# Performance work log

Hardware: AMD Instinct MI355X
Metric: run time of the kernel (lower is better)

## Reference

```python
import jax, jax.numpy as jnp
import numpy as np

T, B, E, H = 2048, 2, 1024, 16
D = E // H  # head_dim = 64

def setup_inputs() -> dict:
    key = jax.random.key(0)
    ks = jax.random.split(key, 9)
    s = 1.0 / np.sqrt(E)
    return {
        "query": jax.random.normal(ks[0], (T, B, E), dtype=jnp.float32),
        "Wq": jax.random.normal(ks[1], (E, E), dtype=jnp.float32) * s,
        "bq": jax.random.normal(ks[2], (E,), dtype=jnp.float32) * 0.02,
        "Wk": jax.random.normal(ks[3], (E, E), dtype=jnp.float32) * s,
        "bk": jax.random.normal(ks[4], (E,), dtype=jnp.float32) * 0.02,
        "Wv": jax.random.normal(ks[5], (E, E), dtype=jnp.float32) * s,
        "bv": jax.random.normal(ks[6], (E,), dtype=jnp.float32) * 0.02,
        "Wo": jax.random.normal(ks[7], (E, E), dtype=jnp.float32) * s,
        "bo": jax.random.normal(ks[8], (E,), dtype=jnp.float32) * 0.02,
    }

def reference(query, Wq, bq, Wk, bk, Wv, bv, Wo, bo):
    # query: [T, B, E] (fairseq Time x Batch x Channel layout)
    t, b, e = query.shape
    scaling = D ** -0.5
    q = (query @ Wq.T + bq) * scaling          # [T,B,E], scaled like fairseq
    k = query @ Wk.T + bk                      # self-attention: k,v from query
    v = query @ Wv.T + bv
    # split heads: [T,B,H,D]
    q = q.reshape(t, b, H, D)
    k = k.reshape(t, b, H, D)
    v = v.reshape(t, b, H, D)
    # attn weights: [B,H,T(tgt),S(src)]
    scores = jnp.einsum("tbhd,sbhd->bhts", q, k)
    probs = jax.nn.softmax(scores, axis=-1)
    # attend: [T,B,H,D] -> [T,B,E]
    ctx = jnp.einsum("bhts,sbhd->tbhd", probs, v).reshape(t, b, e)
    return ctx @ Wo.T + bo                     # [T,B,E]
```

## Files before the change

kernel.cpp:

```cpp
#include <hip/hip_runtime.h>
#include <hip/hip_bf16.h>
#include <math.h>

#define TT 2048
#define BB 2
#define EE 1024
#define HH 16
#define DD 64
#define RR (TT*BB)

typedef __bf16 bf16x8 __attribute__((ext_vector_type(8)));
typedef float  floatx4 __attribute__((ext_vector_type(4)));

__device__ __forceinline__ unsigned short f2b(float f) {
    union { float f; unsigned u; } x{f};
    return (unsigned short)((x.u + 0x7FFFu + ((x.u >> 16) & 1u)) >> 16);
}
__device__ __forceinline__ float b2f_lo(unsigned u) {
    union { unsigned u; float f; } x{u << 16}; return x.f;
}
__device__ __forceinline__ float b2f_hi(unsigned u) {
    union { unsigned u; float f; } x{u & 0xffff0000u}; return x.f;
}

__device__ __forceinline__ float exp2_fast(float x) {
    return __builtin_amdgcn_exp2f(x);
}

typedef const __attribute__((address_space(1))) unsigned int as1_u32;
typedef __attribute__((address_space(3))) unsigned int as3_u32;
__device__ __forceinline__ void gload16(const void* g, void* l) {
    __builtin_amdgcn_global_load_lds((as1_u32*)g, (as3_u32*)l, 16, 0, 0);
}

#define SCALE_Q 0.18033688011112042f

__device__ __forceinline__ int swz(int r) {
    return (r & 7) ^ (((r >> 3) & 3) << 1);
}

__global__ __launch_bounds__(256)
void pack_bf16(const float* __restrict__ x,  const float* __restrict__ wq,
               const float* __restrict__ wk, const float* __restrict__ wv,
               const float* __restrict__ wo, unsigned short* __restrict__ base,
               unsigned short* __restrict__ wob)
{
    const size_t M4 = (size_t)4 << 20, M7 = (size_t)7 << 20;
    const size_t e0 = ((size_t)blockIdx.x * 256 + threadIdx.x) * 8;
    const float* src;
    unsigned short* dst;
    if (e0 < M4) {
        src = x + e0; dst = base + e0;
    } else if (e0 < M7) {
        const int seg = (int)((e0 >> 20) - 4);
        const float* wsrc[3] = {wq, wk, wv};
        src = wsrc[seg] + (e0 & ((1u << 20) - 1));
        dst = base + e0;
    } else {
        src = wo + (e0 - M7); dst = wob + (e0 - M7);
    }
    const float4 a = *(const float4*)src;
    const float4 b = *(const float4*)(src + 4);
    union { unsigned short u[8]; uint4 v; } p;
    p.u[0] = f2b(a.x); p.u[1] = f2b(a.y); p.u[2] = f2b(a.z); p.u[3] = f2b(a.w);
    p.u[4] = f2b(b.x); p.u[5] = f2b(b.y); p.u[6] = f2b(b.z); p.u[7] = f2b(b.w);
    *(uint4*)dst = p.v;
}

template<int MODE>
__global__ __launch_bounds__(256)
void gemm_mfma(const unsigned short* __restrict__ A,
               const unsigned short* __restrict__ Bw,
               const float* __restrict__ b0, const float* __restrict__ b1,
               const float* __restrict__ b2,
               void* __restrict__ out0, void* __restrict__ out1,
               void* __restrict__ out2)
{
    constexpr int BM = 128;
    constexpr int BN = (MODE == 0) ? 128 : 64;
    constexpr int MT = 4;
    constexpr int NT = (MODE == 0) ? 4 : 2;
    constexpr int RA = BM / 32;
    constexpr int RB = BN / 32;
    constexpr int ABYTES = BM * 128;
    constexpr int BUFB   = (BM + BN) * 128;
    __shared__ __align__(16) unsigned char smem[2 * BUFB];

    const int tid  = threadIdx.x;
    const int w    = tid >> 6;
    const int lane = tid & 63;
    const int quad = lane >> 4;
    const int l15  = lane & 15;
    const int wm   = w & 1;
    const int wn   = w >> 1;
    const int i0   = blockIdx.x * BM;
    const int j0   = blockIdx.y * BN;

    const unsigned short* ga[RA];
    const unsigned short* gb[RB];
    #pragma unroll
    for (int r = 0; r < RA; ++r) {
        const int slot = r * 256 + tid;
        const int row  = slot >> 3;
        const int gc   = (slot & 7) ^ swz(row);
        ga[r] = A + (size_t)(i0 + row) * EE + gc * 8;
    }
    #pragma unroll
    for (int r = 0; r < RB; ++r) {
        const int slot = r * 256 + tid;
        const int row  = slot >> 3;
        const int gc   = (slot & 7) ^ swz(row);
        gb[r] = Bw + (size_t)(j0 + row) * EE + gc * 8;
    }

    int ofsA[2][MT], ofsB[2][NT];
    #pragma unroll
    for (int mt = 0; mt < MT; ++mt) {
        const int row = wm * 64 + mt * 16 + l15;
        #pragma unroll
        for (int ks = 0; ks < 2; ++ks)
            ofsA[ks][mt] = row * 64 + (((ks * 4 + quad) ^ swz(row)) << 3);
    }
    #pragma unroll
    for (int nt = 0; nt < NT; ++nt) {
        const int col = wn * (BN / 2) + nt * 16 + l15;
        #pragma unroll
        for (int ks = 0; ks < 2; ++ks)
            ofsB[ks][nt] = col * 64 + (((ks * 4 + quad) ^ swz(col)) << 3);
    }

    floatx4 acc[MT][NT];
    #pragma unroll
    for (int mt = 0; mt < MT; ++mt)
        #pragma unroll
        for (int nt = 0; nt < NT; ++nt)
            acc[mt][nt] = (floatx4){0.f, 0.f, 0.f, 0.f};

    {
        unsigned short* nA = (unsigned short*)(smem);
        unsigned short* nB = (unsigned short*)(smem + ABYTES);
        #pragma unroll
        for (int r = 0; r < RA; ++r)
            gload16(ga[r], nA + (r * 256 + w * 64) * 8);
        #pragma unroll
        for (int r = 0; r < RB; ++r)
            gload16(gb[r], nB + (r * 256 + w * 64) * 8);
    }

    int cur = 0;
    for (int kk = 0; kk < EE; kk += 64) {
        asm volatile("s_waitcnt vmcnt(0)" ::: "memory");
        __builtin_amdgcn_s_barrier();

        if (kk + 64 < EE) {
            unsigned short* nA = (unsigned short*)(smem + (cur ^ 1) * BUFB);
            unsigned short* nB = (unsigned short*)(smem + (cur ^ 1) * BUFB + ABYTES);
            #pragma unroll
            for (int r = 0; r < RA; ++r)
                gload16(ga[r] + kk + 64, nA + (r * 256 + w * 64) * 8);
            #pragma unroll
            for (int r = 0; r < RB; ++r)
                gload16(gb[r] + kk + 64, nB + (r * 256 + w * 64) * 8);
        }
        __builtin_amdgcn_sched_barrier(0);

        const unsigned short* lA = (const unsigned short*)(smem + cur * BUFB);
        const unsigned short* lB = (const unsigned short*)(smem + cur * BUFB + ABYTES);

        bf16x8 af[2][MT], bfr[2][NT];
        #pragma unroll
        for (int ks = 0; ks < 2; ++ks) {
            #pragma unroll
            for (int mt = 0; mt < MT; ++mt)
                af[ks][mt] = __builtin_bit_cast(bf16x8, *(const uint4*)&lA[ofsA[ks][mt]]);
            #pragma unroll
            for (int nt = 0; nt < NT; ++nt)
                bfr[ks][nt] = __builtin_bit_cast(bf16x8, *(const uint4*)&lB[ofsB[ks][nt]]);
        }

        #pragma unroll
        for (int ks = 0; ks < 2; ++ks)
            #pragma unroll
            for (int mt = 0; mt < MT; ++mt)
                #pragma unroll
                for (int nt = 0; nt < NT; ++nt)
                    acc[mt][nt] = __builtin_amdgcn_mfma_f32_16x16x32_bf16(
                        af[ks][mt], bfr[ks][nt], acc[mt][nt], 0, 0, 0);

        cur ^= 1;
    }

    if (MODE == 1) {
        float* dst = (float*)out0;
        #pragma unroll
        for (int nt = 0; nt < NT; ++nt) {
            const int j = j0 + wn * 32 + nt * 16 + l15;
            const float bb = b0[j];
            #pragma unroll
            for (int mt = 0; mt < MT; ++mt) {
                const int i = i0 + wm * 64 + mt * 16 + quad * 4;
                #pragma unroll
                for (int r2 = 0; r2 < 4; ++r2)
                    dst[(size_t)(i + r2) * EE + j] = acc[mt][nt][r2] + bb;
            }
        }
    } else {
        const int which = j0 >> 10;
        const float scale = (which == 0) ? SCALE_Q : 1.0f;
        const float* bias = (which == 0) ? b0 : (which == 1) ? b1 : b2;
        if (which < 2) {
            unsigned short* dst = (unsigned short*)(which == 0 ? out0 : out1);
            #pragma unroll
            for (int nt = 0; nt < NT; ++nt) {
                const int j = (j0 & 1023) + wn * 64 + nt * 16 + l15;
                const int h = j >> 6, d = j & 63;
                const float bb = bias[j];
                #pragma unroll
                for (int mt = 0; mt < MT; ++mt) {
                    const int i = i0 + wm * 64 + mt * 16 + quad * 4;
                    #pragma unroll
                    for (int r2 = 0; r2 < 4; ++r2) {
                        const int ii = i + r2;
                        const int t = ii >> 1, b = ii & 1;
                        dst[((size_t)(b * HH + h) * TT + t) * DD + d] =
                            f2b((acc[mt][nt][r2] + bb) * scale);
                    }
                }
            }
        } else {
            __syncthreads();
            unsigned short* tr = (unsigned short*)smem + (size_t)w * 64 * 68;
            #pragma unroll
            for (int nt = 0; nt < NT; ++nt) {
                const int jl = nt * 16 + l15;
                const float bb = bias[(j0 & 1023) + wn * 64 + jl];
                #pragma unroll
                for (int mt = 0; mt < MT; ++mt) {
                    const int il0 = mt * 16 + quad * 4;
                    ushort4 h4;
                    h4.x = f2b(acc[mt][nt][0] + bb);
                    h4.y = f2b(acc[mt][nt][1] + bb);
                    h4.z = f2b(acc[mt][nt][2] + bb);
                    h4.w = f2b(acc[mt][nt][3] + bb);
                    *(ushort4*)&tr[jl * 68 + il0] = h4;
                }
            }
            __syncthreads();
            const int jg = (j0 & 1023) + wn * 64 + lane;
            const int h = jg >> 6, d = jg & 63;
            const int tb = (i0 + wm * 64) >> 1;
            const unsigned short* rp = tr + (size_t)lane * 68;
            unsigned short* dstV = (unsigned short*)out2;
            #pragma unroll
            for (int g = 0; g < 4; ++g) {
                union { unsigned short u[8]; uint4 v; } pe, po;
                #pragma unroll
                for (int k = 0; k < 8; ++k) {
                    pe.u[k] = rp[(g * 8 + k) * 2];
                    po.u[k] = rp[(g * 8 + k) * 2 + 1];
                }
                *(uint4*)&dstV[((size_t)(0 * HH + h) * DD + d) * TT + tb + g * 8] = pe.v;
                *(uint4*)&dstV[((size_t)(1 * HH + h) * DD + d) * TT + tb + g * 8] = po.v;
            }
        }
    }
}

__global__ __launch_bounds__(256)
void attn_mfma(const unsigned short* __restrict__ Q,
               const unsigned short* __restrict__ K,
               const unsigned short* __restrict__ Vt,
               unsigned short* __restrict__ cpart,
               float* __restrict__ lsumbuf)
{
    __shared__ __align__(16) unsigned short ring[3][2][64 * 64];

    const int tid  = threadIdx.x;
    const int w    = tid >> 6;
    const int lane = tid & 63;
    const int quad = lane >> 4;
    const int l15  = lane & 15;
    const int bh   = blockIdx.x;
    const int tt   = blockIdx.y;
    const int half = blockIdx.z;

    const unsigned short* Qh = Q  + (size_t)bh * TT * DD;
    const unsigned short* Kh = K  + (size_t)bh * TT * DD;
    const unsigned short* Vh = Vt + (size_t)bh * DD * TT;

    const int q0w  = tt * 128 + w * 32;
    const int key0 = half * 1024;

    bf16x8 qf[2][2];
    #pragma unroll
    for (int qn = 0; qn < 2; ++qn)
        #pragma unroll
        for (int kd = 0; kd < 2; ++kd)
            qf[qn][kd] = __builtin_bit_cast(bf16x8,
                *(const uint4*)&Qh[(size_t)(q0w + qn * 16 + l15) * DD + kd * 32 + quad * 8]);

    const unsigned short* kg[4];
    #pragma unroll
    for (int r = 0; r < 4; ++r) {
        const int slot = r * 256 + tid;
        const int row  = slot >> 3;
        const int gc   = (slot & 7) ^ swz(row);
        kg[r] = Kh + (size_t)(key0 + row) * DD + gc * 8;
    }
    const unsigned short* vg[4];
    #pragma unroll
    for (int r = 0; r < 4; ++r) {
        const int s512 = (r & 1) * 256 + tid;
        const int rowd = s512 >> 3;
        const int gc   = (s512 & 7) ^ swz(rowd);
        vg[r] = Vh + (size_t)rowd * TT + key0 + (r >> 1) * 64 + gc * 8;
    }

    int ofsKA[4][2], ofsVB[4][2];
    #pragma unroll
    for (int mt = 0; mt < 4; ++mt) {
        const int row = ((mt >> 1) << 5) + ((l15 >> 2) << 3) + ((mt & 1) << 2) + (l15 & 3);
        #pragma unroll
        for (int kd = 0; kd < 2; ++kd)
            ofsKA[mt][kd] = row * 64 + (((kd * 4 + quad) ^ swz(row)) << 3);
    }
    #pragma unroll
    for (int dn = 0; dn < 4; ++dn) {
        const int row = dn * 16 + l15;
        #pragma unroll
        for (int ks = 0; ks < 2; ++ks)
            ofsVB[dn][ks] = row * 64 + (((ks * 4 + quad) ^ swz(row)) << 3);
    }

    floatx4 cacc[4][2];
    #pragma unroll
    for (int dn = 0; dn < 4; ++dn)
        #pragma unroll
        for (int qn = 0; qn < 2; ++qn)
            cacc[dn][qn] = (floatx4){0.f, 0.f, 0.f, 0.f};
    float rs[2] = {0.f, 0.f};

#define STAGE_ATTN(s)  do {                                                     \
        const int p_ = (s) & 1;                                                 \
        const size_t ko_ = (size_t)((s) >> 1) * 128;                            \
        unsigned short* kd_ = &ring[(s) % 3][0][0];                             \
        unsigned short* vd_ = &ring[(s) % 3][1][0];                             \
        gload16(kg[2 * p_]     + ko_ * DD, kd_ + (size_t)(0 * 256 + w * 64) * 8); \
        gload16(kg[2 * p_ + 1] + ko_ * DD, kd_ + (size_t)(1 * 256 + w * 64) * 8); \
        gload16(vg[2 * p_]     + ko_,      vd_ + (size_t)(0 * 256 + w * 64) * 8); \
        gload16(vg[2 * p_ + 1] + ko_,      vd_ + (size_t)(1 * 256 + w * 64) * 8); \
    } while (0)

    STAGE_ATTN(0);
    STAGE_ATTN(1);

    #pragma unroll
    for (int step = 0; step < 16; ++step) {
        const int rb = step % 3;
        if (step < 15) asm volatile("s_waitcnt vmcnt(4)" ::: "memory");
        else           asm volatile("s_waitcnt vmcnt(0)" ::: "memory");
        __builtin_amdgcn_s_barrier();
        if (step + 2 < 16) STAGE_ATTN(step + 2);
        __builtin_amdgcn_sched_barrier(0);
        __builtin_amdgcn_s_setprio(1);

        const unsigned short* ksub = &ring[rb][0][0];
        const unsigned short* vsub = &ring[rb][1][0];

        uint2 pk[4][2];
        #pragma unroll
        for (int mt = 0; mt < 4; ++mt) {
            const bf16x8 ka0 = __builtin_bit_cast(bf16x8, *(const uint4*)&ksub[ofsKA[mt][0]]);
            const bf16x8 ka1 = __builtin_bit_cast(bf16x8, *(const uint4*)&ksub[ofsKA[mt][1]]);
            #pragma unroll
            for (int qn = 0; qn < 2; ++qn) {
                floatx4 s = (floatx4){0.f, 0.f, 0.f, 0.f};
                s = __builtin_amdgcn_mfma_f32_16x16x32_bf16(ka0, qf[qn][0], s, 0, 0, 0);
                s = __builtin_amdgcn_mfma_f32_16x16x32_bf16(ka1, qf[qn][1], s, 0, 0, 0);
                const float p0 = exp2_fast(s[0]);
                const float p1 = exp2_fast(s[1]);
                const float p2 = exp2_fast(s[2]);
                const float p3 = exp2_fast(s[3]);
                rs[qn] += (p0 + p1) + (p2 + p3);
                union { __hip_bfloat162 h2[2]; uint2 u; } c;
                c.h2[0] = __float22bfloat162_rn(make_float2(p0, p1));
                c.h2[1] = __float22bfloat162_rn(make_float2(p2, p3));
                pk[mt][qn] = c.u;
            }
        }
        bf16x8 pa[2][2];
        #pragma unroll
        for (int qn = 0; qn < 2; ++qn) {
            union { uint2 d[2]; uint4 v; } a0, a1;
            a0.d[0] = pk[0][qn]; a0.d[1] = pk[1][qn];
            a1.d[0] = pk[2][qn]; a1.d[1] = pk[3][qn];
            pa[qn][0] = __builtin_bit_cast(bf16x8, a0.v);
            pa[qn][1] = __builtin_bit_cast(bf16x8, a1.v);
        }
        #pragma unroll
        for (int dn = 0; dn < 4; ++dn) {
            const bf16x8 vb0 = __builtin_bit_cast(bf16x8, *(const uint4*)&vsub[ofsVB[dn][0]]);
            const bf16x8 vb1 = __builtin_bit_cast(bf16x8, *(const uint4*)&vsub[ofsVB[dn][1]]);
            #pragma unroll
            for (int qn = 0; qn < 2; ++qn) {
                cacc[dn][qn] = __builtin_amdgcn_mfma_f32_16x16x32_bf16(pa[qn][0], vb0, cacc[dn][qn], 0, 0, 0);
                cacc[dn][qn] = __builtin_amdgcn_mfma_f32_16x16x32_bf16(pa[qn][1], vb1, cacc[dn][qn], 0, 0, 0);
            }
        }
        __builtin_amdgcn_s_setprio(0);
    }
#undef STAGE_ATTN

    const int b = bh / HH, hh = bh % HH;
    float rsw[2];
    #pragma unroll
    for (int qn = 0; qn < 2; ++qn) {
        float t = rs[qn];
        t += __shfl_xor(t, 16);
        t += __shfl_xor(t, 32);
        rsw[qn] = t;
    }
    unsigned short* cp = cpart + (size_t)half * RR * EE;
    #pragma unroll
    for (int qn = 0; qn < 2; ++qn) {
        #pragma unroll
        for (int dn = 0; dn < 4; ++dn) {
            const int e = hh * 64 + dn * 16 + l15;
            #pragma unroll
            for (int j = 0; j < 4; ++j) {
                const int t = q0w + qn * 16 + quad * 4 + j;
                cp[(size_t)(t * BB + b) * EE + e] = f2b(cacc[dn][qn][j]);
            }
        }
    }
    if (quad == 0) {
        lsumbuf[(half * BB * HH + bh) * TT + q0w + 0 * 16 + l15] = rsw[0];
        lsumbuf[(half * BB * HH + bh) * TT + q0w + 1 * 16 + l15] = rsw[1];
    }
}

__global__ __launch_bounds__(256)
void combine(const unsigned short* __restrict__ cpart,
             const float* __restrict__ lsumbuf,
             unsigned short* __restrict__ cb)
{
    const int gid = blockIdx.x * 256 + threadIdx.x;
    const int e0 = (gid & 127) * 8;
    const int r  = gid >> 7;
    const int t = r >> 1, b = r & 1;
    const int h = e0 >> 6;
    const int bh = b * HH + h;
    const float inv = 1.0f /
        (lsumbuf[bh * TT + t] + lsumbuf[(BB * HH + bh) * TT + t]);
    const uint4 c0 = *(const uint4*)&cpart[(size_t)r * EE + e0];
    const uint4 c1 = *(const uint4*)&cpart[(size_t)RR * EE + (size_t)r * EE + e0];
    const unsigned u0[4] = {c0.x, c0.y, c0.z, c0.w};
    const unsigned u1[4] = {c1.x, c1.y, c1.z, c1.w};
    union { unsigned u[4]; uint4 v; } o;
    #pragma unroll
    for (int k = 0; k < 4; ++k) {
        const float lo = (b2f_lo(u0[k]) + b2f_lo(u1[k])) * inv;
        const float hi = (b2f_hi(u0[k]) + b2f_hi(u1[k])) * inv;
        union { __hip_bfloat162 h2; unsigned u; } pk;
        pk.h2 = __float22bfloat162_rn(make_float2(lo, hi));
        o.u[k] = pk.u;
    }
    *(uint4*)&cb[(size_t)r * EE + e0] = o.v;
}

extern "C" void kernel_launch(void* const* d_in, const int* in_sizes, int n_in,
                              void* d_out, int out_size, void* d_ws, size_t ws_size,
                              hipStream_t stream)
{
    const float* x  = (const float*)d_in[0];
    const float* Wq = (const float*)d_in[1];
    const float* bq = (const float*)d_in[2];
    const float* Wk = (const float*)d_in[3];
    const float* bk = (const float*)d_in[4];
    const float* Wv = (const float*)d_in[5];
    const float* bv = (const float*)d_in[6];
    const float* Wo = (const float*)d_in[7];
    const float* bo = (const float*)d_in[8];
    float* out = (float*)d_out;

    const size_t M1 = (size_t)1 << 20;
    unsigned short* base  = (unsigned short*)d_ws;
    unsigned short* xb    = base;
    unsigned short* wqkv  = base + 4 * M1;
    unsigned short* cpart = base;
    unsigned short* qb    = base + 8 * M1;
    unsigned short* kb    = base + 12 * M1;
    unsigned short* vtb   = base + 16 * M1;
    unsigned short* cb    = base + 20 * M1;
    unsigned short* wob   = base + 24 * M1;
    float*          lsum  = (float*)(base + 25 * M1);

    dim3 blk(256);

    pack_bf16<<<dim3(4096), blk, 0, stream>>>(x, Wq, Wk, Wv, Wo, base, wob);

    gemm_mfma<0><<<dim3(RR / 128, 3072 / 128), blk, 0, stream>>>(
        xb, wqkv, bq, bk, bv, qb, kb, vtb);

    attn_mfma<<<dim3(BB * HH, TT / 128, 2), blk, 0, stream>>>(qb, kb, vtb, cpart, lsum);

    combine<<<dim3(RR * EE / 8 / 256), blk, 0, stream>>>(cpart, lsum, cb);

    gemm_mfma<1><<<dim3(RR / 128, EE / 64), blk, 0, stream>>>(
        cb, wob, bo, nullptr, nullptr, out, nullptr, nullptr);
}
```

Measured before the change: 179.9 us.

## Drop split-KV attention and fuse normalization into attention epilogue

Each attention block now walks all 2048 keys instead of half, and the separate combine kernel and partial-output buffers are removed. The softmax normalization by the row sum happens in the attention epilogue through lane shuffles before the bf16 store. This removes one launch plus the write and reread of two partial context tensors. The cost is half as many attention blocks (512 instead of 1024), so fewer waves are available to fill the GPU's compute units.

```diff
diff --git a/kernel.cpp b/kernel.cpp
--- a/kernel.cpp
+++ b/kernel.cpp
@@ -270,8 +270,7 @@
 void attn_mfma(const unsigned short* __restrict__ Q,
                const unsigned short* __restrict__ K,
                const unsigned short* __restrict__ Vt,
-               unsigned short* __restrict__ cpart,
-               float* __restrict__ lsumbuf)
+               unsigned short* __restrict__ cb)
 {
     __shared__ __align__(16) unsigned short ring[3][2][64 * 64];
 
@@ -282,14 +281,12 @@
     const int l15  = lane & 15;
     const int bh   = blockIdx.x;
     const int tt   = blockIdx.y;
-    const int half = blockIdx.z;
 
     const unsigned short* Qh = Q  + (size_t)bh * TT * DD;
     const unsigned short* Kh = K  + (size_t)bh * TT * DD;
     const unsigned short* Vh = Vt + (size_t)bh * DD * TT;
 
     const int q0w  = tt * 128 + w * 32;
-    const int key0 = half * 1024;
 
     bf16x8 qf[2][2];
     #pragma unroll
@@ -305,7 +302,7 @@
         const int slot = r * 256 + tid;
         const int row  = slot >> 3;
         const int gc   = (slot & 7) ^ swz(row);
-        kg[r] = Kh + (size_t)(key0 + row) * DD + gc * 8;
+        kg[r] = Kh + (size_t)row * DD + gc * 8;
     }
     const unsigned short* vg[4];
     #pragma unroll
@@ -313,7 +310,7 @@
         const int s512 = (r & 1) * 256 + tid;
         const int rowd = s512 >> 3;
         const int gc   = (s512 & 7) ^ swz(rowd);
-        vg[r] = Vh + (size_t)rowd * TT + key0 + (r >> 1) * 64 + gc * 8;
+        vg[r] = Vh + (size_t)rowd * TT + (r >> 1) * 64 + gc * 8;
     }
 
     int ofsKA[4][2], ofsVB[4][2];
@@ -355,12 +352,12 @@
     STAGE_ATTN(1);
 
     #pragma unroll
-    for (int step = 0; step < 16; ++step) {
+    for (int step = 0; step < 32; ++step) {
         const int rb = step % 3;
-        if (step < 15) asm volatile("s_waitcnt vmcnt(4)" ::: "memory");
+        if (step < 31) asm volatile("s_waitcnt vmcnt(4)" ::: "memory");
         else           asm volatile("s_waitcnt vmcnt(0)" ::: "memory");
         __builtin_amdgcn_s_barrier();
-        if (step + 2 < 16) STAGE_ATTN(step + 2);
+        if (step + 2 < 32) STAGE_ATTN(step + 2);
         __builtin_amdgcn_sched_barrier(0);
         __builtin_amdgcn_s_setprio(1);
 
@@ -412,60 +409,30 @@
 #undef STAGE_ATTN
 
     const int b = bh / HH, hh = bh % HH;
-    float rsw[2];
+    float invv[2];
     #pragma unroll
     for (int qn = 0; qn < 2; ++qn) {
         float t = rs[qn];
         t += __shfl_xor(t, 16);
         t += __shfl_xor(t, 32);
-        rsw[qn] = t;
-    }
-    unsigned short* cp = cpart + (size_t)half * RR * EE;
+        invv[qn] = 1.0f / t;
+    }
     #pragma unroll
     for (int qn = 0; qn < 2; ++qn) {
+        float invq[4];
+        #pragma unroll
+        for (int j = 0; j < 4; ++j)
+            invq[j] = __shfl(invv[qn], quad * 4 + j);
         #pragma unroll
         for (int dn = 0; dn < 4; ++dn) {
             const int e = hh * 64 + dn * 16 + l15;
             #pragma unroll
             for (int j = 0; j < 4; ++j) {
                 const int t = q0w + qn * 16 + quad * 4 + j;
-                cp[(size_t)(t * BB + b) * EE + e] = f2b(cacc[dn][qn][j]);
-            }
-        }
-    }
-    if (quad == 0) {
-        lsumbuf[(half * BB * HH + bh) * TT + q0w + 0 * 16 + l15] = rsw[0];
-        lsumbuf[(half * BB * HH + bh) * TT + q0w + 1 * 16 + l15] = rsw[1];
-    }
-}
-
-__global__ __launch_bounds__(256)
-void combine(const unsigned short* __restrict__ cpart,
-             const float* __restrict__ lsumbuf,
-             unsigned short* __restrict__ cb)
-{
-    const int gid = blockIdx.x * 256 + threadIdx.x;
-    const int e0 = (gid & 127) * 8;
-    const int r  = gid >> 7;
-    const int t = r >> 1, b = r & 1;
-    const int h = e0 >> 6;
-    const int bh = b * HH + h;
-    const float inv = 1.0f /
-        (lsumbuf[bh * TT + t] + lsumbuf[(BB * HH + bh) * TT + t]);
-    const uint4 c0 = *(const uint4*)&cpart[(size_t)r * EE + e0];
-    const uint4 c1 = *(const uint4*)&cpart[(size_t)RR * EE + (size_t)r * EE + e0];
-    const unsigned u0[4] = {c0.x, c0.y, c0.z, c0.w};
-    const unsigned u1[4] = {c1.x, c1.y, c1.z, c1.w};
-    union { unsigned u[4]; uint4 v; } o;
-    #pragma unroll
-    for (int k = 0; k < 4; ++k) {
-        const float lo = (b2f_lo(u0[k]) + b2f_lo(u1[k])) * inv;
-        const float hi = (b2f_hi(u0[k]) + b2f_hi(u1[k])) * inv;
-        union { __hip_bfloat162 h2; unsigned u; } pk;
-        pk.h2 = __float22bfloat162_rn(make_float2(lo, hi));
-        o.u[k] = pk.u;
-    }
-    *(uint4*)&cb[(size_t)r * EE + e0] = o.v;
+                cb[(size_t)(t * BB + b) * EE + e] = f2b(cacc[dn][qn][j] * invq[j]);
+            }
+        }
+    }
 }
 
 extern "C" void kernel_launch(void* const* d_in, const int* in_sizes, int n_in,
@@ -487,13 +454,11 @@
     unsigned short* base  = (unsigned short*)d_ws;
     unsigned short* xb    = base;
     unsigned short* wqkv  = base + 4 * M1;
-    unsigned short* cpart = base;
     unsigned short* qb    = base + 8 * M1;
     unsigned short* kb    = base + 12 * M1;
     unsigned short* vtb   = base + 16 * M1;
     unsigned short* cb    = base + 20 * M1;
     unsigned short* wob   = base + 24 * M1;
-    float*          lsum  = (float*)(base + 25 * M1);
 
     dim3 blk(256);
 
@@ -502,9 +467,7 @@
     gemm_mfma<0><<<dim3(RR / 128, 3072 / 128), blk, 0, stream>>>(
         xb, wqkv, bq, bk, bv, qb, kb, vtb);
 
-    attn_mfma<<<dim3(BB * HH, TT / 128, 2), blk, 0, stream>>>(qb, kb, vtb, cpart, lsum);
-
-    combine<<<dim3(RR * EE / 8 / 256), blk, 0, stream>>>(cpart, lsum, cb);
+    attn_mfma<<<dim3(BB * HH, TT / 128), blk, 0, stream>>>(qb, kb, vtb, cb);
 
     gemm_mfma<1><<<dim3(RR / 128, EE / 64), blk, 0, stream>>>(
         cb, wob, bo, nullptr, nullptr, out, nullptr, nullptr);
```

Result: slower. 392.4 us (+118.1%).
